# Kernel tuning notes

Measured on AMD Instinct MI355X. Metric: run time of the kernel, lower is better.

The kernel has to match this reference:

```python
import jax, jax.numpy as jnp
import numpy as np

B, C, H, W = 32, 128, 32, 32
E, K, D, HID = 16, 2, 128, 512  # nbExperts, topK, nbIn=nbOut, hidden=4*max(nbIn,nbOut)


def setup_inputs() -> dict:
    key = jax.random.key(0)
    ks = jax.random.split(key, 6)
    init = lambda k, shape, fan: (jax.random.normal(k, shape, jnp.float32) / np.sqrt(fan)).astype(jnp.float32)
    return {
        "x": jax.random.normal(ks[0], (B, C, H, W), jnp.float32),
        "gate_w": init(ks[1], (D, E), D),
        "gate_b": jnp.zeros((E,), jnp.float32),
        "noise_w": init(ks[2], (D, E), D),
        "noise_b": jnp.zeros((E,), jnp.float32),
        "w1": init(ks[3], (E, D, HID), D),
        "b1": jnp.zeros((E, HID), jnp.float32),
        "w2": init(ks[4], (E, HID, D), HID),
        "b2": jnp.zeros((E, D), jnp.float32),
        "top_k": K,
    }


def reference(x, gate_w, gate_b, noise_w, noise_b, w1, b1, w2, b2, top_k):
    b, c, h, w = x.shape
    xt = x.transpose(0, 2, 3, 1).reshape(-1, c)  # [T, D] tokens (fromCNN path)
    T = xt.shape[0]

    # --- GatingWithNoise: gate(x) + randn * softplus(noise(x)) ---
    logits = xt @ gate_w + gate_b                      # [T, E]
    noise_sd = jax.nn.softplus(xt @ noise_w + noise_b)  # [T, E]
    noise = jax.random.normal(jax.random.key(42), logits.shape, logits.dtype)
    logits = logits + noise * noise_sd

    # --- top-k, softmax over k, scatter to dense [T, E] gate matrix ---
    top_vals, top_idx = jax.lax.top_k(logits, top_k)   # [T, K]
    probs = jax.nn.softmax(top_vals, axis=1)           # [T, K]
    gates = jnp.zeros((T, E), x.dtype).at[jnp.arange(T)[:, None], top_idx].set(probs)

    # --- dense path: run every expert, weighted combine ---
    hdn = jax.nn.relu(jnp.einsum('td,edh->teh', xt, w1) + b1)  # [T, E, HID]
    eo = jnp.einsum('teh,ehd->ted', hdn, w2) + b2              # [T, E, D]
    out = jnp.einsum('te,ted->td', gates, eo)                  # [T, D]

    out = out.reshape(b, h, w, c).transpose(0, 3, 1, 2)        # back to NCHW
    gates = gates.reshape(b, h, w, E)
    return out, gates
```

## Files before the change

kernel.cpp:

```cpp
#include <hip/hip_runtime.h>
#include <stdint.h>

#define NB       32
#define NC       128
#define NHW      1024
#define NT       32768
#define NE       16
#define NHID     512
#define NGBLK    512

typedef __attribute__((ext_vector_type(8))) short short8v;
typedef __attribute__((ext_vector_type(4))) float f32x4;

__device__ __forceinline__ unsigned short f2bf(float f) {
    uint32_t u = __float_as_uint(f);
    uint32_t r = u + 0x7fffu + ((u >> 16) & 1u);
    return (unsigned short)(r >> 16);
}
__device__ __forceinline__ float bf2f(unsigned short u) {
    return __uint_as_float(((uint32_t)u) << 16);
}

__device__ __forceinline__ void gll16(const void* g, void* l) {
    __builtin_amdgcn_global_load_lds(
        (const __attribute__((address_space(1))) uint32_t*)g,
        (__attribute__((address_space(3))) uint32_t*)l, 16, 0, 0);
}

#define WAIT_VMLGKM() asm volatile("s_waitcnt vmcnt(0) lgkmcnt(0)" ::: "memory")
#define WAIT_LGKM()   asm volatile("s_waitcnt lgkmcnt(0)" ::: "memory")
#define SBAR()        { asm volatile("" ::: "memory"); __builtin_amdgcn_s_barrier(); asm volatile("" ::: "memory"); }

__device__ __forceinline__ uint32_t rotl32(uint32_t x, uint32_t d) {
    return (x << d) | (x >> (32u - d));
}

__device__ __forceinline__ void threefry2x32_20(uint32_t k0, uint32_t k1,
                                                uint32_t& x0, uint32_t& x1) {
    const uint32_t ks0 = k0, ks1 = k1, ks2 = k0 ^ k1 ^ 0x1BD11BDAu;
    x0 += ks0; x1 += ks1;
#define TFR(r) { x0 += x1; x1 = rotl32(x1, r); x1 ^= x0; }
    TFR(13u) TFR(15u) TFR(26u) TFR(6u)
    x0 += ks1; x1 += ks2 + 1u;
    TFR(17u) TFR(29u) TFR(16u) TFR(24u)
    x0 += ks2; x1 += ks0 + 2u;
    TFR(13u) TFR(15u) TFR(26u) TFR(6u)
    x0 += ks0; x1 += ks1 + 3u;
    TFR(17u) TFR(29u) TFR(16u) TFR(24u)
    x0 += ks1; x1 += ks2 + 4u;
    TFR(13u) TFR(15u) TFR(26u) TFR(6u)
    x0 += ks2; x1 += ks0 + 5u;
#undef TFR
}

__device__ __forceinline__ float erfinv_xla_f32(float x) {
    float w = -log1pf(-x * x);
    float p;
    if (w < 5.0f) {
        w = w - 2.5f;
        p = 2.81022636e-08f;
        p = fmaf(p, w, 3.43273939e-07f);
        p = fmaf(p, w, -3.5233877e-06f);
        p = fmaf(p, w, -4.39150654e-06f);
        p = fmaf(p, w, 0.00021858087f);
        p = fmaf(p, w, -0.00125372503f);
        p = fmaf(p, w, -0.00417768164f);
        p = fmaf(p, w, 0.246640727f);
        p = fmaf(p, w, 1.50140941f);
    } else {
        w = sqrtf(w) - 3.0f;
        p = -0.000200214257f;
        p = fmaf(p, w, 0.000100950558f);
        p = fmaf(p, w, 0.00134934322f);
        p = fmaf(p, w, -0.00367342844f);
        p = fmaf(p, w, 0.00573950773f);
        p = fmaf(p, w, -0.0076224613f);
        p = fmaf(p, w, 0.00943887047f);
        p = fmaf(p, w, 1.00167406f);
        p = fmaf(p, w, 2.83297682f);
    }
    return p * x;
}

__device__ __forceinline__ float jax_noise_elem(uint32_t i) {
    uint32_t x0 = 0u, x1 = i;
    threefry2x32_20(0u, 42u, x0, x1);
    uint32_t bits = x0 ^ x1;
    float f = __uint_as_float(0x3f800000u | (bits >> 9)) - 1.0f;
    const float lo = -0.99999994f;
    float u = f * 2.0f + lo;
    u = fmaxf(lo, u);
    return 1.41421354f * erfinv_xla_f32(u);
}

__global__ __launch_bounds__(256) void moe_gate_kernel(
    const float* __restrict__ x,
    const float* __restrict__ gate_w, const float* __restrict__ gate_b,
    const float* __restrict__ noise_w, const float* __restrict__ noise_b,
    float* __restrict__ gates_out,
    int*   __restrict__ top_idx,
    float* __restrict__ top_prob,
    int*   __restrict__ rank,
    int*   __restrict__ bcnt,
    unsigned short* __restrict__ xtb,
    int do_new)
{
    __shared__ float lw[32 * 160];
    __shared__ int   lcnt[16];

    const int tid = threadIdx.x;
    const int tl  = tid >> 2;
    const int q   = tid & 3;
    const int t   = blockIdx.x * 64 + tl;
    const int b   = t >> 10, hw = t & 1023;

    if (tid < 16) lcnt[tid] = 0;

    for (int idx = tid; idx < 4096; idx += 256) {
        int ci = idx >> 7;
        int r  = idx & 127;
        int qq = r >> 5, e = r & 31;
        int c  = qq * 32 + ci;
        float v = (e < 16) ? gate_w[c * 16 + e] : noise_w[c * 16 + (e - 16)];
        lw[ci * 160 + qq * 40 + e] = v;
    }
    __syncthreads();

    float acc[32];
    #pragma unroll
    for (int e = 0; e < 32; ++e) acc[e] = 0.f;

    unsigned short xh[32];
    const float* xq = x + (size_t)b * (NC * NHW) + (size_t)(q * 32) * NHW + hw;
    const float* wq = lw + q * 40;
    #pragma unroll 4
    for (int ci = 0; ci < 32; ++ci) {
        float xv = xq[(size_t)ci << 10];
        xh[ci] = f2bf(xv);
        const f32x4* wr = (const f32x4*)(wq + ci * 160);
        #pragma unroll
        for (int j = 0; j < 8; ++j) {
            f32x4 w4 = wr[j];
            #pragma unroll
            for (int k = 0; k < 4; ++k)
                acc[j * 4 + k] = fmaf(xv, w4[k], acc[j * 4 + k]);
        }
    }

    if (do_new) {
        #pragma unroll
        for (int j = 0; j < 4; ++j) {
            short8v v;
            #pragma unroll
            for (int k = 0; k < 8; ++k) v[k] = (short)xh[j * 8 + k];
            *(short8v*)(xtb + (size_t)t * 128 + q * 32 + j * 8) = v;
        }
    }

    #pragma unroll
    for (int e = 0; e < 32; ++e) {
        acc[e] += __shfl_xor(acc[e], 1);
        acc[e] += __shfl_xor(acc[e], 2);
    }

    float lg[4];
    #pragma unroll
    for (int j = 0; j < 4; ++j) {
        int e = q * 4 + j;
        float g  = acc[e] + gate_b[e];
        float an = acc[16 + e] + noise_b[e];
        float sd = fmaxf(an, 0.f) + log1pf(expf(-fabsf(an)));
        float nz = jax_noise_elem((uint32_t)t * 16u + (uint32_t)e);
        lg[j] = fmaf(nz, sd, g);
    }

    float v1 = lg[0], v2 = -INFINITY;
    int   i1 = q * 4, i2 = 0x7fffffff;
    #pragma unroll
    for (int j = 1; j < 4; ++j) {
        float v = lg[j]; int e = q * 4 + j;
        if (v > v1) { v2 = v1; i2 = i1; v1 = v; i1 = e; }
        else if (v > v2) { v2 = v; i2 = e; }
    }
    #pragma unroll
    for (int m = 1; m <= 2; m <<= 1) {
        float pv1 = __shfl_xor(v1, m), pv2 = __shfl_xor(v2, m);
        int   pi1 = __shfl_xor(i1, m), pi2 = __shfl_xor(i2, m);
        bool pBest = (pv1 > v1) || (pv1 == v1 && pi1 < i1);
        float c2v; int c2i;
        if (pBest) { c2v = v1;  c2i = i1;  v1 = pv1; i1 = pi1;
                     if (!((c2v > pv2) || (c2v == pv2 && c2i < pi2))) { c2v = pv2; c2i = pi2; }
        } else     { c2v = pv1; c2i = pi1;
                     if (!((c2v > v2)  || (c2v == v2  && c2i < i2)))  { c2v = v2;  c2i = i2;  }
        }
        v2 = c2v; i2 = c2i;
    }

    float qq = expf(v2 - v1);
    float s  = 1.0f + qq;
    float p1 = 1.0f / s;
    float p2 = qq / s;

    f32x4 g4;
    #pragma unroll
    for (int j = 0; j < 4; ++j) {
        int e = q * 4 + j;
        g4[j] = (e == i1) ? p1 : ((e == i2) ? p2 : 0.f);
    }
    *(f32x4*)(gates_out + (size_t)t * 16 + q * 4) = g4;

    if (q == 0) {
        top_idx[t * 2 + 0] = i1;  top_idx[t * 2 + 1] = i2;
        top_prob[t * 2 + 0] = p1; top_prob[t * 2 + 1] = p2;
        if (do_new) {
            int r1 = atomicAdd(&lcnt[i1], 1);
            int r2 = atomicAdd(&lcnt[i2], 1);
            rank[t * 2 + 0] = r1;
            rank[t * 2 + 1] = r2;
        }
    }
    if (do_new) {
        __syncthreads();
        if (tid < 16) bcnt[blockIdx.x * 16 + tid] = lcnt[tid];
    }
}

__global__ __launch_bounds__(256) void transpose_convert2_kernel(
    const float* __restrict__ w1, unsigned short* __restrict__ w1bt,
    const float* __restrict__ w2, unsigned short* __restrict__ w2bt)
{
    __shared__ float ts[64][65];
    int blk = blockIdx.x;
    const float* src;  unsigned short* dst;  int R, C;
    if (blk < 256) { src = w1; dst = w1bt; R = 128; C = 512; }
    else           { src = w2; dst = w2bt; R = 512; C = 128; blk -= 256; }
    const int nr = R >> 6, ncc = C >> 6;
    const int e = blk / (nr * ncc);
    const int rem = blk % (nr * ncc);
    const int rt = rem / ncc, ct = rem % ncc;
    const float* S = src + (size_t)e * R * C + (size_t)(rt * 64) * C + ct * 64;
    unsigned short* D = dst + (size_t)e * R * C + (size_t)(ct * 64) * R + rt * 64;
    const int tid = threadIdx.x;
    #pragma unroll
    for (int i = 0; i < 16; ++i) {
        int lin = i * 256 + tid;
        int r = lin >> 6, c = lin & 63;
        ts[r][c] = S[(size_t)r * C + c];
    }
    __syncthreads();
    #pragma unroll
    for (int i = 0; i < 16; ++i) {
        int lin = i * 256 + tid;
        int c = lin >> 6, r = lin & 63;
        D[(size_t)c * R + r] = f2bf(ts[r][c]);
    }
}

__global__ __launch_bounds__(256) void scan_kernel(
    const int* __restrict__ bcnt,
    int* __restrict__ poff, int* __restrict__ blk2e,
    int* __restrict__ blk2chunk, int* __restrict__ total_chunks,
    int* __restrict__ bbase,
    int* __restrict__ pair_tok)
{
    __shared__ int ps[16][17];
    __shared__ int gb[16][17];
    __shared__ int scnt[16];
    __shared__ int snch[16];
    __shared__ int scum[17];
    __shared__ int spoff[16];
    const int tid = threadIdx.x;
    const int e = tid >> 4, g = tid & 15;

    int s = 0;
    for (int b = g * 32; b < g * 32 + 32; ++b)
        s += bcnt[b * 16 + e];
    ps[e][g] = s;
    __syncthreads();

    if (tid < 16) {
        int run = 0;
        for (int gg = 0; gg < 16; ++gg) { gb[tid][gg] = run; run += ps[tid][gg]; }
        scnt[tid] = run;
        snch[tid] = (run + 127) >> 7;
    }
    __syncthreads();

    if (tid == 0) {
        int cc = 0, off = 0;
        for (int ee = 0; ee < 16; ++ee) {
            scum[ee] = cc; spoff[ee] = off;
            cc += snch[ee]; off += snch[ee] << 7;
        }
        scum[16] = cc;
        *total_chunks = cc;
    }
    __syncthreads();
    const int tot = scum[16];
    for (int idx = tid; idx < tot; idx += 256) {
        int ee = 0;
        #pragma unroll
        for (int k = 0; k < 15; ++k)
            if (idx >= scum[k + 1]) ee = k + 1;
        blk2e[idx] = ee;
        blk2chunk[idx] = idx - scum[ee];
    }
    if (tid < 16) poff[tid] = spoff[tid];

    {
        int run = spoff[e] + gb[e][g];
        for (int b = g * 32; b < g * 32 + 32; ++b) {
            bbase[b * 16 + e] = run;
            run += bcnt[b * 16 + e];
        }
    }

    for (int ee = 0; ee < 16; ++ee) {
        int start = spoff[ee] + scnt[ee];
        int end   = spoff[ee] + (snch[ee] << 7);
        for (int i = start + tid; i < end; i += 256)
            pair_tok[i] = -1;
    }
}

__global__ __launch_bounds__(256) void scatter_kernel(
    const int* __restrict__ top_idx, const int* __restrict__ rank,
    const int* __restrict__ bbase, int* __restrict__ pair_tok,
    int* __restrict__ slot_of)
{
    int i = blockIdx.x * 256 + threadIdx.x;
    int t = i >> 1;
    int e = top_idx[i];
    int slot = bbase[(t >> 6) * 16 + e] + rank[i];
    pair_tok[slot] = t;
    slot_of[i] = slot;
}

__device__ __forceinline__ void stage_w1(const unsigned short* w1e, short* W1s,
                                         int hcn, int wid, int lane) {
    #pragma unroll
    for (int k2 = 0; k2 < 2; ++k2) {
        int i2 = wid * 2 + k2;
        int r2 = i2 * 4 + (lane >> 4);
        int s2 = lane & 15;
        gll16(w1e + (size_t)(hcn + r2) * 128 + ((s2 ^ (r2 & 15)) * 8),
              W1s + i2 * 512);
    }
}
__device__ __forceinline__ void stage_w2(const unsigned short* w2e, short* W2s,
                                         int hcn, int wid, int lane) {
    #pragma unroll
    for (int k2 = 0; k2 < 2; ++k2) {
        int i2 = wid * 2 + k2;
        int r2 = i2 * 8 + (lane >> 3);
        int s2 = lane & 7;
        gll16(w2e + (size_t)r2 * 512 + hcn + ((s2 ^ (r2 & 7)) * 8),
              W2s + i2 * 512);
    }
}

__global__ __launch_bounds__(512, 4) void moe_mfma_kernel(
    const unsigned short* __restrict__ xtb,
    const int* __restrict__ pair_tok, const int* __restrict__ blk2e,
    const int* __restrict__ blk2chunk, const int* __restrict__ poff,
    const int* __restrict__ total_chunks,
    const unsigned short* __restrict__ w1bt,
    const float* __restrict__ b1,
    const unsigned short* __restrict__ w2bt,
    const float* __restrict__ b2,
    unsigned short* __restrict__ pair_y)
{
    __shared__ short Xs[128 * 128];
    __shared__ short Hs[128 * 64];
    __shared__ short W1s[64 * 128];
    __shared__ short W2s[128 * 64];

    const int blk = blockIdx.x;
    if (blk >= *total_chunks) return;
    const int e  = blk2e[blk];
    const int p0 = poff[e] + (blk2chunk[blk] << 7);
    const int tid  = threadIdx.x;
    const int lane = tid & 63;
    const int wid  = tid >> 6;
    const int wm   = wid >> 1;
    const int wn   = wid & 1;
    const int l16  = lane & 15;
    const int lg   = lane >> 4;

    const unsigned short* w1e = w1bt + (size_t)e * 512 * 128;
    const unsigned short* w2e = w2bt + (size_t)e * 128 * 512;

    stage_w1(w1e, W1s, 0, wid, lane);
    stage_w2(w2e, W2s, 0, wid, lane);

    #pragma unroll
    for (int i = 0; i < 4; ++i) {
        int lin = i * 512 + tid;
        int row = lin >> 4, kc = lin & 15;
        int tok = pair_tok[p0 + row];
        short8v v = {};
        if (tok >= 0)
            v = *(const short8v*)(xtb + (size_t)tok * 128 + kc * 8);
        *(short8v*)(Xs + row * 128 + ((kc ^ (row & 15)) * 8)) = v;
    }

    f32x4 yacc[2][4];
    #pragma unroll
    for (int mi = 0; mi < 2; ++mi)
        #pragma unroll
        for (int ni = 0; ni < 4; ++ni)
            yacc[mi][ni] = (f32x4){0.f, 0.f, 0.f, 0.f};

    const int rowA0 = wm * 32 + l16, rowA1 = rowA0 + 16;

    for (int c = 0; c < 8; ++c) {
        WAIT_VMLGKM(); SBAR();

        f32x4 hacc[2][2];
        #pragma unroll
        for (int mi = 0; mi < 2; ++mi)
            #pragma unroll
            for (int ni = 0; ni < 2; ++ni)
                hacc[mi][ni] = (f32x4){0.f, 0.f, 0.f, 0.f};

        #pragma unroll
        for (int kk = 0; kk < 4; ++kk) {
            int slot = kk * 4 + lg;
            short8v a0 = *(const short8v*)(Xs + rowA0 * 128 + ((slot ^ (rowA0 & 15)) * 8));
            short8v a1 = *(const short8v*)(Xs + rowA1 * 128 + ((slot ^ (rowA1 & 15)) * 8));
            #pragma unroll
            for (int ni = 0; ni < 2; ++ni) {
                int hr = wn * 32 + ni * 16 + l16;
                short8v bfr = *(const short8v*)(W1s + hr * 128 + ((slot ^ (hr & 15)) * 8));
                hacc[0][ni] = __builtin_amdgcn_mfma_f32_16x16x32_bf16(a0, bfr, hacc[0][ni], 0, 0, 0);
                hacc[1][ni] = __builtin_amdgcn_mfma_f32_16x16x32_bf16(a1, bfr, hacc[1][ni], 0, 0, 0);
            }
        }
        #pragma unroll
        for (int ni = 0; ni < 2; ++ni) {
            int col = wn * 32 + ni * 16 + l16;
            float b1v = b1[e * 512 + (c << 6) + col];
            #pragma unroll
            for (int mi = 0; mi < 2; ++mi) {
                #pragma unroll
                for (int r = 0; r < 4; ++r) {
                    int m = wm * 32 + mi * 16 + lg * 4 + r;
                    float v = fmaxf(hacc[mi][ni][r] + b1v, 0.f);
                    Hs[m * 64 + (((col >> 3) ^ (m & 7)) << 3) + (col & 7)] = (short)f2bf(v);
                }
            }
        }
        WAIT_LGKM(); SBAR();

        if (c < 7) stage_w1(w1e, W1s, (c + 1) << 6, wid, lane);

        #pragma unroll
        for (int kk = 0; kk < 2; ++kk) {
            int slot = kk * 4 + lg;
            short8v a0 = *(const short8v*)(Hs + rowA0 * 64 + ((slot ^ (rowA0 & 7)) * 8));
            short8v a1 = *(const short8v*)(Hs + rowA1 * 64 + ((slot ^ (rowA1 & 7)) * 8));
            #pragma unroll
            for (int ni = 0; ni < 4; ++ni) {
                int dr = wn * 64 + ni * 16 + l16;
                short8v bfr = *(const short8v*)(W2s + dr * 64 + ((slot ^ (dr & 7)) * 8));
                yacc[0][ni] = __builtin_amdgcn_mfma_f32_16x16x32_bf16(a0, bfr, yacc[0][ni], 0, 0, 0);
                yacc[1][ni] = __builtin_amdgcn_mfma_f32_16x16x32_bf16(a1, bfr, yacc[1][ni], 0, 0, 0);
            }
        }
        WAIT_LGKM(); SBAR();

        if (c < 7) stage_w2(w2e, W2s, (c + 1) << 6, wid, lane);
    }

    #pragma unroll
    for (int ni = 0; ni < 4; ++ni) {
        int d = wn * 64 + ni * 16 + l16;
        float b2v = b2[e * 128 + d];
        #pragma unroll
        for (int mi = 0; mi < 2; ++mi) {
            #pragma unroll
            for (int r = 0; r < 4; ++r) {
                int m = wm * 32 + mi * 16 + lg * 4 + r;
                pair_y[(size_t)(p0 + m) * 128 + d] = f2bf(yacc[mi][ni][r] + b2v);
            }
        }
    }
}

__global__ __launch_bounds__(256) void combine_kernel(
    const unsigned short* __restrict__ pair_y, const int* __restrict__ slot_of,
    const float* __restrict__ top_prob, float* __restrict__ out)
{
    __shared__ float ob[64][129];
    const int blk = blockIdx.x;
    const int b = blk >> 4;
    const int hw0 = (blk & 15) << 6;
    const int tid = threadIdx.x;
    #pragma unroll
    for (int i = 0; i < 4; ++i) {
        int lin = i * 256 + tid;
        int tl = lin >> 4, dg = lin & 15;
        int t = b * 1024 + hw0 + tl;
        int s0 = slot_of[t * 2], s1 = slot_of[t * 2 + 1];
        float p0 = top_prob[t * 2], p1 = top_prob[t * 2 + 1];
        short8v y0 = *(const short8v*)(pair_y + (size_t)s0 * 128 + dg * 8);
        short8v y1 = *(const short8v*)(pair_y + (size_t)s1 * 128 + dg * 8);
        #pragma unroll
        for (int j = 0; j < 8; ++j)
            ob[tl][dg * 8 + j] = p0 * bf2f((unsigned short)y0[j]) + p1 * bf2f((unsigned short)y1[j]);
    }
    __syncthreads();
    #pragma unroll
    for (int i = 0; i < 32; ++i) {
        int lin = i * 256 + tid;
        int d = lin >> 6, hwl = lin & 63;
        out[((size_t)b * 128 + d) * 1024 + hw0 + hwl] = ob[hwl][d];
    }
}

__global__ __launch_bounds__(256) void moe_expert_kernel(
    const float* __restrict__ x,
    const int* __restrict__ top_idx, const float* __restrict__ top_prob,
    const float* __restrict__ w1, const float* __restrict__ b1,
    const float* __restrict__ w2, const float* __restrict__ b2,
    float* __restrict__ out)
{
    __shared__ float xsB[128];
    __shared__ float hb[512];

    const int tid = threadIdx.x;
    const int t = blockIdx.x;
    const int b = t >> 10, hw = t & 1023;

    if (tid < 128)
        xsB[tid] = x[((size_t)b * 128 + tid) * NHW + hw];
    __syncthreads();

    float oacc = 0.f;
    #pragma unroll
    for (int k = 0; k < 2; ++k) {
        const int e = top_idx[t * 2 + k];
        const float pw = top_prob[t * 2 + k];
        const float* W1 = w1 + (size_t)e * (128 * 512);
        float a0 = 0.f, a1 = 0.f;
        for (int d = 0; d < 128; ++d) {
            float xv = xsB[d];
            a0 = fmaf(xv, W1[d * 512 + tid], a0);
            a1 = fmaf(xv, W1[d * 512 + tid + 256], a1);
        }
        hb[tid]       = fmaxf(a0 + b1[e * 512 + tid], 0.f);
        hb[tid + 256] = fmaxf(a1 + b1[e * 512 + tid + 256], 0.f);
        __syncthreads();
        if (tid < 128) {
            const float* W2 = w2 + (size_t)e * (512 * 128);
            float a = 0.f;
            for (int h = 0; h < 512; ++h)
                a = fmaf(hb[h], W2[h * 128 + tid], a);
            oacc = fmaf(pw, a + b2[e * 128 + tid], oacc);
        }
        __syncthreads();
    }
    if (tid < 128)
        out[((size_t)b * 128 + tid) * NHW + hw] = oacc;
}

extern "C" void kernel_launch(void* const* d_in, const int* in_sizes, int n_in,
                              void* d_out, int out_size, void* d_ws, size_t ws_size,
                              hipStream_t stream) {
    const float* x       = (const float*)d_in[0];
    const float* gate_w  = (const float*)d_in[1];
    const float* gate_b  = (const float*)d_in[2];
    const float* noise_w = (const float*)d_in[3];
    const float* noise_b = (const float*)d_in[4];
    const float* w1      = (const float*)d_in[5];
    const float* b1      = (const float*)d_in[6];
    const float* w2      = (const float*)d_in[7];
    const float* b2      = (const float*)d_in[8];

    float* out   = (float*)d_out;
    float* gates = out + (size_t)NB * NC * NHW;

    const size_t OFF_POFF   = 0;
    const size_t OFF_TOTAL  = 1024;
    const size_t OFF_B2E    = 4096;
    const size_t OFF_B2C    = 8192;
    const size_t OFF_TIDX   = 12288;
    const size_t OFF_RANK   = OFF_TIDX  + (size_t)NT * 2 * 4;
    const size_t OFF_SLOT   = OFF_RANK  + (size_t)NT * 2 * 4;
    const size_t OFF_PROB   = OFF_SLOT  + (size_t)NT * 2 * 4;
    const size_t OFF_BCNT   = OFF_PROB  + (size_t)NT * 2 * 4;
    const size_t OFF_BBASE  = OFF_BCNT  + (size_t)NGBLK * 16 * 4;
    const size_t OFF_XTB    = OFF_BBASE + (size_t)NGBLK * 16 * 4;
    const size_t OFF_W1BT   = OFF_XTB   + (size_t)NT * 128 * 2;
    const size_t OFF_W2BT   = OFF_W1BT  + (size_t)NE * 512 * 128 * 2;
    const size_t OFF_PTOK   = OFF_W2BT  + (size_t)NE * 128 * 512 * 2;
    const size_t NPAIR_PAD  = 67584;
    const size_t OFF_PAIRY  = OFF_PTOK  + NPAIR_PAD * 4;
    const size_t NEED       = OFF_PAIRY + NPAIR_PAD * 128 * 2;

    char* ws = (char*)d_ws;
    int*   poff     = (int*)(ws + OFF_POFF);
    int*   total_ch = (int*)(ws + OFF_TOTAL);
    int*   blk2e    = (int*)(ws + OFF_B2E);
    int*   blk2c    = (int*)(ws + OFF_B2C);
    int*   top_idx  = (int*)(ws + OFF_TIDX);
    int*   rank     = (int*)(ws + OFF_RANK);
    int*   slot_of  = (int*)(ws + OFF_SLOT);
    float* top_prob = (float*)(ws + OFF_PROB);
    int*   bcnt     = (int*)(ws + OFF_BCNT);
    int*   bbase    = (int*)(ws + OFF_BBASE);
    unsigned short* xtb    = (unsigned short*)(ws + OFF_XTB);
    unsigned short* w1bt   = (unsigned short*)(ws + OFF_W1BT);
    unsigned short* w2bt   = (unsigned short*)(ws + OFF_W2BT);
    int*   pair_tok = (int*)(ws + OFF_PTOK);
    unsigned short* pair_y = (unsigned short*)(ws + OFF_PAIRY);

    const int use_new = (ws_size >= NEED) ? 1 : 0;

    moe_gate_kernel<<<NT / 64, 256, 0, stream>>>(
        x, gate_w, gate_b, noise_w, noise_b,
        gates, top_idx, top_prob, rank, bcnt, xtb, use_new);

    if (use_new) {
        transpose_convert2_kernel<<<512, 256, 0, stream>>>(w1, w1bt, w2, w2bt);
        scan_kernel<<<1, 256, 0, stream>>>(bcnt, poff, blk2e, blk2c, total_ch,
                                           bbase, pair_tok);
        scatter_kernel<<<NT * 2 / 256, 256, 0, stream>>>(top_idx, rank, bbase,
                                                         pair_tok, slot_of);
        moe_mfma_kernel<<<528, 512, 0, stream>>>(
            xtb, pair_tok, blk2e, blk2c, poff, total_ch,
            w1bt, b1, w2bt, b2, pair_y);
        combine_kernel<<<512, 256, 0, stream>>>(pair_y, slot_of, top_prob, out);
    } else {
        moe_expert_kernel<<<NT, 256, 0, stream>>>(
            x, top_idx, top_prob, w1, b1, w2, b2, out);
    }
}
```

Measured before the change: 95.64 us.

## Fuse weight transpose into gate kernel, remap MFMA blocks, relax vmcnt waits

```diff
diff --git a/kernel.cpp b/kernel.cpp
--- a/kernel.cpp
+++ b/kernel.cpp
@@ -27,9 +27,11 @@
         (__attribute__((address_space(3))) uint32_t*)l, 16, 0, 0);
 }
 
-#define WAIT_VMLGKM() asm volatile("s_waitcnt vmcnt(0) lgkmcnt(0)" ::: "memory")
-#define WAIT_LGKM()   asm volatile("s_waitcnt lgkmcnt(0)" ::: "memory")
-#define SBAR()        { asm volatile("" ::: "memory"); __builtin_amdgcn_s_barrier(); asm volatile("" ::: "memory"); }
+#define WAIT_VM2_LGKM0() asm volatile("s_waitcnt vmcnt(2) lgkmcnt(0)" ::: "memory")
+#define WAIT_VM2()       asm volatile("s_waitcnt vmcnt(2)" ::: "memory")
+#define WAIT_VM0()       asm volatile("s_waitcnt vmcnt(0)" ::: "memory")
+#define WAIT_LGKM()      asm volatile("s_waitcnt lgkmcnt(0)" ::: "memory")
+#define SBAR()           { asm volatile("" ::: "memory"); __builtin_amdgcn_s_barrier(); asm volatile("" ::: "memory"); }
 
 __device__ __forceinline__ uint32_t rotl32(uint32_t x, uint32_t d) {
     return (x << d) | (x >> (32u - d));
@@ -93,7 +95,7 @@
     return 1.41421354f * erfinv_xla_f32(u);
 }
 
-__global__ __launch_bounds__(256) void moe_gate_kernel(
+__global__ __launch_bounds__(256) void moe_gate_tw_kernel(
     const float* __restrict__ x,
     const float* __restrict__ gate_w, const float* __restrict__ gate_b,
     const float* __restrict__ noise_w, const float* __restrict__ noise_b,
@@ -103,12 +105,42 @@
     int*   __restrict__ rank,
     int*   __restrict__ bcnt,
     unsigned short* __restrict__ xtb,
+    const float* __restrict__ w1, unsigned short* __restrict__ w1bt,
+    const float* __restrict__ w2, unsigned short* __restrict__ w2bt,
     int do_new)
 {
-    __shared__ float lw[32 * 160];
-    __shared__ int   lcnt[16];
+    __shared__ union { float lw[32 * 160]; float ts[64][65]; } sm;
+    __shared__ int lcnt[16];
 
     const int tid = threadIdx.x;
+
+    if (blockIdx.x >= NGBLK) {
+        int blk = blockIdx.x - NGBLK;
+        const float* src;  unsigned short* dst;  int R, C;
+        if (blk < 256) { src = w1; dst = w1bt; R = 128; C = 512; }
+        else           { src = w2; dst = w2bt; R = 512; C = 128; blk -= 256; }
+        const int nr = R >> 6, ncc = C >> 6;
+        const int e = blk / (nr * ncc);
+        const int rem = blk % (nr * ncc);
+        const int rt = rem / ncc, ct = rem % ncc;
+        const float* S = src + (size_t)e * R * C + (size_t)(rt * 64) * C + ct * 64;
+        unsigned short* D = dst + (size_t)e * R * C + (size_t)(ct * 64) * R + rt * 64;
+        #pragma unroll
+        for (int i = 0; i < 16; ++i) {
+            int lin = i * 256 + tid;
+            int r = lin >> 6, c = lin & 63;
+            sm.ts[r][c] = S[(size_t)r * C + c];
+        }
+        __syncthreads();
+        #pragma unroll
+        for (int i = 0; i < 16; ++i) {
+            int lin = i * 256 + tid;
+            int c = lin >> 6, r = lin & 63;
+            D[(size_t)c * R + r] = f2bf(sm.ts[r][c]);
+        }
+        return;
+    }
+
     const int tl  = tid >> 2;
     const int q   = tid & 3;
     const int t   = blockIdx.x * 64 + tl;
@@ -122,7 +154,7 @@
         int qq = r >> 5, e = r & 31;
         int c  = qq * 32 + ci;
         float v = (e < 16) ? gate_w[c * 16 + e] : noise_w[c * 16 + (e - 16)];
-        lw[ci * 160 + qq * 40 + e] = v;
+        sm.lw[ci * 160 + qq * 40 + e] = v;
     }
     __syncthreads();
 
@@ -132,7 +164,7 @@
 
     unsigned short xh[32];
     const float* xq = x + (size_t)b * (NC * NHW) + (size_t)(q * 32) * NHW + hw;
-    const float* wq = lw + q * 40;
+    const float* wq = sm.lw + q * 40;
     #pragma unroll 4
     for (int ci = 0; ci < 32; ++ci) {
         float xv = xq[(size_t)ci << 10];
@@ -222,37 +254,6 @@
     if (do_new) {
         __syncthreads();
         if (tid < 16) bcnt[blockIdx.x * 16 + tid] = lcnt[tid];
-    }
-}
-
-__global__ __launch_bounds__(256) void transpose_convert2_kernel(
-    const float* __restrict__ w1, unsigned short* __restrict__ w1bt,
-    const float* __restrict__ w2, unsigned short* __restrict__ w2bt)
-{
-    __shared__ float ts[64][65];
-    int blk = blockIdx.x;
-    const float* src;  unsigned short* dst;  int R, C;
-    if (blk < 256) { src = w1; dst = w1bt; R = 128; C = 512; }
-    else           { src = w2; dst = w2bt; R = 512; C = 128; blk -= 256; }
-    const int nr = R >> 6, ncc = C >> 6;
-    const int e = blk / (nr * ncc);
-    const int rem = blk % (nr * ncc);
-    const int rt = rem / ncc, ct = rem % ncc;
-    const float* S = src + (size_t)e * R * C + (size_t)(rt * 64) * C + ct * 64;
-    unsigned short* D = dst + (size_t)e * R * C + (size_t)(ct * 64) * R + rt * 64;
-    const int tid = threadIdx.x;
-    #pragma unroll
-    for (int i = 0; i < 16; ++i) {
-        int lin = i * 256 + tid;
-        int r = lin >> 6, c = lin & 63;
-        ts[r][c] = S[(size_t)r * C + c];
-    }
-    __syncthreads();
-    #pragma unroll
-    for (int i = 0; i < 16; ++i) {
-        int lin = i * 256 + tid;
-        int c = lin >> 6, r = lin & 63;
-        D[(size_t)c * R + r] = f2bf(ts[r][c]);
     }
 }
 
@@ -375,7 +376,7 @@
     __shared__ short W1s[64 * 128];
     __shared__ short W2s[128 * 64];
 
-    const int blk = blockIdx.x;
+    const int blk = (blockIdx.x & 7) * 66 + (blockIdx.x >> 3);
     if (blk >= *total_chunks) return;
     const int e  = blk2e[blk];
     const int p0 = poff[e] + (blk2chunk[blk] << 7);
@@ -414,7 +415,7 @@
     const int rowA0 = wm * 32 + l16, rowA1 = rowA0 + 16;
 
     for (int c = 0; c < 8; ++c) {
-        WAIT_VMLGKM(); SBAR();
+        WAIT_VM2_LGKM0(); SBAR();
 
         f32x4 hacc[2][2];
         #pragma unroll
@@ -452,7 +453,9 @@
         }
         WAIT_LGKM(); SBAR();
 
-        if (c < 7) stage_w1(w1e, W1s, (c + 1) << 6, wid, lane);
+        if (c < 7) { stage_w1(w1e, W1s, (c + 1) << 6, wid, lane); WAIT_VM2(); }
+        else       { WAIT_VM0(); }
+        SBAR();
 
         #pragma unroll
         for (int kk = 0; kk < 2; ++kk) {
@@ -617,12 +620,12 @@
 
     const int use_new = (ws_size >= NEED) ? 1 : 0;
 
-    moe_gate_kernel<<<NT / 64, 256, 0, stream>>>(
+    moe_gate_tw_kernel<<<use_new ? (NGBLK + 512) : NGBLK, 256, 0, stream>>>(
         x, gate_w, gate_b, noise_w, noise_b,
-        gates, top_idx, top_prob, rank, bcnt, xtb, use_new);
+        gates, top_idx, top_prob, rank, bcnt, xtb,
+        w1, w1bt, w2, w2bt, use_new);
 
     if (use_new) {
-        transpose_convert2_kernel<<<512, 256, 0, stream>>>(w1, w1bt, w2, w2bt);
         scan_kernel<<<1, 256, 0, stream>>>(bcnt, poff, blk2e, blk2c, total_ch,
                                            bbase, pair_tok);
         scatter_kernel<<<NT * 2 / 256, 256, 0, stream>>>(top_idx, rank, bbase,
```

Result: faster. 92.11 us (-3.7%).
